# Kernel optimization log

Hardware: AMD Instinct MI355X
Metric: run time of the kernel (lower is better)

The kernel has to match this reference:

```python
import jax, jax.numpy as jnp
import numpy as np
from jax import lax

LEAK = 0.2   # LeakyReLU negative slope
EPS = 1e-5   # LayerNorm eps (torch default)
K = 16       # nsample

def _lrelu(x):
    return jnp.where(x > 0, x, LEAK * x)

def _ln(x, g, b):
    m = x.mean(-1, keepdims=True)
    v = x.var(-1, keepdims=True)
    return (x - m) / jnp.sqrt(v + EPS) * g + b

def _pointconv(xyz, new_xyz, feats, W, b):
    # xyz [B,N,3], new_xyz [B,M,3], feats [B,N,C] -> [B,M,O]
    d2 = (jnp.sum(new_xyz**2, -1)[:, :, None]
          + jnp.sum(xyz**2, -1)[:, None, :]
          - 2.0 * jnp.einsum('bmd,bnd->bmn', new_xyz, xyz))   # [B,M,N]
    _, idx = lax.top_k(-d2, K)                                # kNN indices [B,M,K]
    bidx = jnp.arange(xyz.shape[0])[:, None, None]
    g_xyz = xyz[bidx, idx] - new_xyz[:, :, None, :]           # relative coords [B,M,K,3]
    g_f = feats[bidx, idx]                                    # neighbor feats  [B,M,K,C]
    g = jnp.concatenate([g_xyz, g_f], -1)                     # [B,M,K,C+3]
    h = _lrelu(jnp.einsum('bmkc,co->bmko', g, W) + b)         # local MLP
    return h.max(2)                                           # max-pool over neighbors

def setup_inputs():
    key = jax.random.key(0)
    ks = jax.random.split(key, 8)
    B, N, base, C1 = 256, 1024, 16, 32
    def w(k, shape, fan):
        return jax.random.normal(k, shape, jnp.float32) * (1.0 / np.sqrt(fan))
    return dict(
        point_cloud=jax.random.normal(ks[0], (B, 3, N), jnp.float32),
        pw_W0=w(ks[1], (3, base), 3), pw_b0=jnp.zeros(base), pw_g0=jnp.ones(base), pw_beta0=jnp.zeros(base),
        pw_W1=w(ks[2], (base, base), base), pw_b1=jnp.zeros(base), pw_g1=jnp.ones(base), pw_beta1=jnp.zeros(base),
        pc0_W=w(ks[3], (base + 3, C1), base + 3), pc0_b=jnp.zeros(C1),
        bn_Ws=w(ks[4], (C1, C1 // 4), C1), bn_bs=jnp.zeros(C1 // 4),
        bn_Wc=w(ks[5], (C1 // 4 + 3, 128), C1 // 4 + 3), bn_bc=jnp.zeros(128),
        bn_We=w(ks[6], (128, 256), 128), bn_be=jnp.zeros(256),
    )

def reference(point_cloud, pw_W0, pw_b0, pw_g0, pw_beta0, pw_W1, pw_b1, pw_g1, pw_beta1,
              pc0_W, pc0_b, bn_Ws, bn_bs, bn_Wc, bn_bc, bn_We, bn_be):
    xyz0 = jnp.swapaxes(point_cloud, 1, 2)   # [B,1024,3]
    xyz1 = xyz0[:, ::2]                      # strided downsample -> [B,512,3]
    xyz2 = xyz1[:, ::4]                      # -> [B,128,3]
    # pointwise MLP (Linear-LN-LeakyReLU x2)
    f = _lrelu(_ln(xyz0 @ pw_W0 + pw_b0, pw_g0, pw_beta0))
    f = _lrelu(_ln(f @ pw_W1 + pw_b1, pw_g1, pw_beta1))       # [B,1024,16]
    # PointConv layer 0: 1024 -> 512 points, 16 -> 32 ch
    f = _pointconv(xyz0, xyz1, f, pc0_W, pc0_b)               # [B,512,32]
    # BottleneckStridedPointConv: squeeze (32->8), grouped conv (->128), expand (->256)
    fs = _lrelu(f @ bn_Ws + bn_bs)                            # [B,512,8]
    f = _pointconv(xyz1, xyz2, fs, bn_Wc, bn_bc)              # [B,128,128]
    f = f @ bn_We + bn_be                                     # [B,128,256]
    return f.mean(1)                                          # mean over points -> [B,256]
```

## Files before the change

### kernel.cpp

```cpp
#include <hip/hip_runtime.h>
#include <float.h>
#include <math.h>

#define LEAK 0.2f
#define EPS 1e-5f

__device__ __forceinline__ float lrelu(float v){ return v > 0.f ? v : LEAK*v; }

__device__ __forceinline__ void ln_lrelu16(float* h, const float* __restrict__ g, const float* __restrict__ be){
  float mu = 0.f;
#pragma unroll
  for (int o=0;o<16;o++) mu += h[o];
  mu *= 0.0625f;
  float var = 0.f;
#pragma unroll
  for (int o=0;o<16;o++){ float d = h[o]-mu; var += d*d; }
  var *= 0.0625f;
  float rs = 1.0f / sqrtf(var + EPS);
#pragma unroll
  for (int o=0;o<16;o++){ float v = (h[o]-mu)*rs*g[o] + be[o]; h[o] = lrelu(v); }
}

__global__ __launch_bounds__(256) void prep_kernel(const float* __restrict__ pc,
    const float* __restrict__ W0, const float* __restrict__ b0, const float* __restrict__ g0, const float* __restrict__ be0,
    const float* __restrict__ W1, const float* __restrict__ b1, const float* __restrict__ g1, const float* __restrict__ be1,
    float4* __restrict__ cand, float* __restrict__ feats)
{
  const int p = blockIdx.x*256 + threadIdx.x;
  const int b = p >> 10, n = p & 1023;
  const float* base = pc + b*3072;
  const float x = base[n], y = base[1024+n], z = base[2048+n];
  cand[p] = make_float4(x, y, z, x*x + y*y + z*z);
  float h[16];
#pragma unroll
  for (int o=0;o<16;o++) h[o] = b0[o] + x*W0[o] + y*W0[16+o] + z*W0[32+o];
  ln_lrelu16(h, g0, be0);
  float h2[16];
#pragma unroll
  for (int o=0;o<16;o++){
    float s = b1[o];
#pragma unroll
    for (int c=0;c<16;c++) s += h[c]*W1[c*16+o];
    h2[o] = s;
  }
  ln_lrelu16(h2, g1, be1);
  float4* fo = (float4*)(feats + p*16);
  fo[0] = make_float4(h2[0],h2[1],h2[2],h2[3]);
  fo[1] = make_float4(h2[4],h2[5],h2[6],h2[7]);
  fo[2] = make_float4(h2[8],h2[9],h2[10],h2[11]);
  fo[3] = make_float4(h2[12],h2[13],h2[14],h2[15]);
}

#define KNN_SENT 0xFF7FFC00u
__device__ __forceinline__ unsigned enc_key(float d, int n){
  unsigned u = __float_as_uint(d);
  u ^= (unsigned)(((int)u) >> 31) | 0x80000000u;
  return (u & ~1023u) | (unsigned)n;
}
__device__ __forceinline__ float dec_key(unsigned k){
  unsigned u = k ^ ((unsigned)(~(((int)k) >> 31)) | 0x80000000u);
  return __uint_as_float(u);
}

__device__ __forceinline__ unsigned med3u(unsigned a, unsigned b, unsigned c){
  unsigned d;
  asm("v_med3_u32 %0, %1, %2, %3" : "=v"(d) : "v"(a), "v"(b), "v"(c));
  return d;
}

__device__ __forceinline__ void ins_sorted(unsigned (&dk)[16], unsigned key){
#pragma unroll
  for (int j=15;j>0;--j) dk[j] = med3u(dk[j-1], dk[j], key);
  dk[0] = key < dk[0] ? key : dk[0];
}

template<int QS, int CS, int NQTOT, int NQ, int SPLIT, int NCAND>
__device__ __forceinline__ void knn_body(const float4* __restrict__ cand, int* __restrict__ idx_out)
{
  constexpr int NC = NCAND / SPLIT;
  constexpr int QG = NQTOT / NQ;
  constexpr int W  = SPLIT*NQ;
  __shared__ unsigned md[16*W];
  const int b = blockIdx.x / QG, qg = blockIdx.x % QG;
  const int tid = threadIdx.x;
  const int m = tid & (NQ-1), s = tid / NQ;
  const int mg = qg*NQ + m;
  const float4* __restrict__ cb = cand + b*1024;
  const float4 qv = cb[mg*QS];
  const float qx2=-2.f*qv.x, qy2=-2.f*qv.y, qz2=-2.f*qv.z;
  const int n0u = __builtin_amdgcn_readfirstlane(s*NC);

  unsigned dk[16];
#pragma unroll
  for (int j=0;j<16;j++) dk[j] = KNN_SENT;

#pragma unroll
  for (int t=0;t<16;t++){
    float4 c = cb[(n0u+t)*CS];
    float d = fmaf(c.x,qx2, fmaf(c.y,qy2, fmaf(c.z,qz2, c.w)));
    ins_sorted(dk, enc_key(d, n0u+t));
  }
  float Tf = dec_key(dk[15]);

  for (int ch=0; ch<NC/64; ch++){
    const int cb0u = n0u + ch*64;
    unsigned long long msk = 0ull;
    if (ch == 0){
#pragma unroll
      for (int t=16;t<64;t++){
        float4 c = cb[(cb0u+t)*CS];
        float d = fmaf(c.x,qx2, fmaf(c.y,qy2, fmaf(c.z,qz2, c.w)));
        if (d < Tf) msk |= (1ull<<t);
      }
    } else {
#pragma unroll 16
      for (int t=0;t<64;t++){
        float4 c = cb[(cb0u+t)*CS];
        float d = fmaf(c.x,qx2, fmaf(c.y,qy2, fmaf(c.z,qz2, c.w)));
        if (d < Tf) msk |= (1ull<<t);
      }
    }
    while (msk){
      const int t = __builtin_ctzll(msk);
      msk &= msk-1ull;
      float4 c = cb[(cb0u+t)*CS];
      float d = fmaf(c.x,qx2, fmaf(c.y,qy2, fmaf(c.z,qz2, c.w)));
      ins_sorted(dk, enc_key(d, cb0u+t));
    }
    Tf = dec_key(dk[15]);
  }

  if (s > 0){
    const int col = s*NQ + m;
#pragma unroll
    for (int j=0;j<16;j++) md[j*W + col] = dk[j];
  }
#pragma unroll
  for (int step = SPLIT/2; step > 1; step >>= 1){
    __syncthreads();
    if (s < step){
      const int col2 = (s+step)*NQ + m;
#pragma unroll
      for (int j=0;j<16;j++) ins_sorted(dk, md[j*W + col2]);
      if (s > 0){
        const int col = s*NQ + m;
#pragma unroll
        for (int j=0;j<16;j++) md[j*W + col] = dk[j];
      }
    }
  }
  __syncthreads();
  if (s == 0){
    const int col2 = NQ + m;
#pragma unroll
    for (int j=0;j<16;j++){
      unsigned o = md[(15-j)*W + col2];
      dk[j] = o < dk[j] ? o : dk[j];
    }
    int ik[16];
#pragma unroll
    for (int j=0;j<16;j++) ik[j] = (int)(dk[j] & 1023u);
    int4* op = (int4*)(idx_out + (b*NQTOT + mg)*16);
    op[0] = make_int4(ik[0],ik[1],ik[2],ik[3]);
    op[1] = make_int4(ik[4],ik[5],ik[6],ik[7]);
    op[2] = make_int4(ik[8],ik[9],ik[10],ik[11]);
    op[3] = make_int4(ik[12],ik[13],ik[14],ik[15]);
  }
}

__global__ __attribute__((amdgpu_flat_work_group_size(1024,1024), amdgpu_waves_per_eu(4,4)))
void knn1_kernel(const float4* __restrict__ cand, int* __restrict__ idx_out){
  knn_body<2,1,512,512,2,1024>(cand, idx_out);
}
__global__ __attribute__((amdgpu_flat_work_group_size(1024,1024), amdgpu_waves_per_eu(4,4)))
void knn2_kernel(const float4* __restrict__ cand, int* __restrict__ idx_out){
  knn_body<8,2,128,128,8,512>(cand, idx_out);
}

__global__ __attribute__((amdgpu_flat_work_group_size(512,512), amdgpu_waves_per_eu(2,2)))
void feat1_kernel(const float4* __restrict__ cand,
    const float* __restrict__ feats, const int* __restrict__ idx1,
    const float* __restrict__ W, const float* __restrict__ Wb,
    const float* __restrict__ Ws, const float* __restrict__ bs,
    float* __restrict__ fs_out)
{
  __shared__ float sP[1024*32];
  __shared__ float sx[1024], sy[1024], sz[1024];
  const int b = blockIdx.x, tid = threadIdx.x;
  const float4* __restrict__ cb = cand + b*1024;
  { float4 c0 = cb[tid], c1 = cb[tid+512];
    sx[tid]=c0.x; sy[tid]=c0.y; sz[tid]=c0.z;
    sx[tid+512]=c1.x; sy[tid+512]=c1.y; sz[tid+512]=c1.z; }

  const float4* __restrict__ fb4 = (const float4*)(feats + b*16384);
#pragma unroll
  for (int i=0;i<2;i++){
    const int j = tid + i*512;
    float4 f0 = fb4[j*4+0], f1 = fb4[j*4+1], f2 = fb4[j*4+2], f3 = fb4[j*4+3];
    float f[16] = {f0.x,f0.y,f0.z,f0.w, f1.x,f1.y,f1.z,f1.w,
                   f2.x,f2.y,f2.z,f2.w, f3.x,f3.y,f3.z,f3.w};
    float* row = sP + j*32;
    const int sw = (j & 7);
#pragma unroll
    for (int o4=0;o4<8;o4++){
      float4 s = *(const float4*)(Wb + o4*4);
#pragma unroll
      for (int c=0;c<16;c++){
        float4 w = *(const float4*)(W + (3+c)*32 + o4*4);
        s.x = fmaf(f[c], w.x, s.x);
        s.y = fmaf(f[c], w.y, s.y);
        s.z = fmaf(f[c], w.z, s.z);
        s.w = fmaf(f[c], w.w, s.w);
      }
      *(float4*)(row + ((o4 ^ sw) << 2)) = s;
    }
  }
  __syncthreads();

  const int m = tid;
  const float qx = sx[2*m], qy = sy[2*m], qz = sz[2*m];
  int idxr[16];
  { const int4* ip = (const int4*)(idx1 + (b*512+m)*16);
    int4 a=ip[0], b2=ip[1], c2=ip[2], d2=ip[3];
    idxr[0]=a.x; idxr[1]=a.y; idxr[2]=a.z; idxr[3]=a.w;
    idxr[4]=b2.x; idxr[5]=b2.y; idxr[6]=b2.z; idxr[7]=b2.w;
    idxr[8]=c2.x; idxr[9]=c2.y; idxr[10]=c2.z; idxr[11]=c2.w;
    idxr[12]=d2.x; idxr[13]=d2.y; idxr[14]=d2.z; idxr[15]=d2.w; }

  float w0[32], w1[32], w2[32];
#pragma unroll
  for (int o4=0;o4<8;o4++){
    float4 a = *(const float4*)(W +       o4*4);
    float4 bb= *(const float4*)(W + 32  + o4*4);
    float4 cc= *(const float4*)(W + 64  + o4*4);
    w0[o4*4]=a.x; w0[o4*4+1]=a.y; w0[o4*4+2]=a.z; w0[o4*4+3]=a.w;
    w1[o4*4]=bb.x; w1[o4*4+1]=bb.y; w1[o4*4+2]=bb.z; w1[o4*4+3]=bb.w;
    w2[o4*4]=cc.x; w2[o4*4+1]=cc.y; w2[o4*4+2]=cc.z; w2[o4*4+3]=cc.w;
  }

  float acc[32];
#pragma unroll
  for (int o=0;o<32;o++) acc[o] = -FLT_MAX;

#pragma unroll 4
  for (int k=0;k<16;k++){
    const int j = idxr[k];
    const float gx = sx[j]-qx, gy = sy[j]-qy, gz = sz[j]-qz;
    const float* row = sP + j*32;
    const int sw = (j & 7);
#pragma unroll
    for (int o4=0;o4<8;o4++){
      float4 p = *(const float4*)(row + ((o4 ^ sw) << 2));
      const int o0 = o4*4;
      float h0 = fmaf(gz, w2[o0+0], fmaf(gy, w1[o0+0], fmaf(gx, w0[o0+0], p.x)));
      float h1 = fmaf(gz, w2[o0+1], fmaf(gy, w1[o0+1], fmaf(gx, w0[o0+1], p.y)));
      float h2 = fmaf(gz, w2[o0+2], fmaf(gy, w1[o0+2], fmaf(gx, w0[o0+2], p.z)));
      float h3 = fmaf(gz, w2[o0+3], fmaf(gy, w1[o0+3], fmaf(gx, w0[o0+3], p.w)));
      acc[o0+0] = fmaxf(acc[o0+0], fmaxf(h0, 0.2f*h0));
      acc[o0+1] = fmaxf(acc[o0+1], fmaxf(h1, 0.2f*h1));
      acc[o0+2] = fmaxf(acc[o0+2], fmaxf(h2, 0.2f*h2));
      acc[o0+3] = fmaxf(acc[o0+3], fmaxf(h3, 0.2f*h3));
    }
  }

  float fsacc[8] = {0.f,0.f,0.f,0.f,0.f,0.f,0.f,0.f};
#pragma unroll
  for (int o=0;o<32;o++){
    const float a = acc[o];
    float4 u = *(const float4*)(Ws + o*8);
    float4 v = *(const float4*)(Ws + o*8 + 4);
    fsacc[0] = fmaf(a, u.x, fsacc[0]);
    fsacc[1] = fmaf(a, u.y, fsacc[1]);
    fsacc[2] = fmaf(a, u.z, fsacc[2]);
    fsacc[3] = fmaf(a, u.w, fsacc[3]);
    fsacc[4] = fmaf(a, v.x, fsacc[4]);
    fsacc[5] = fmaf(a, v.y, fsacc[5]);
    fsacc[6] = fmaf(a, v.z, fsacc[6]);
    fsacc[7] = fmaf(a, v.w, fsacc[7]);
  }
  float r[8];
#pragma unroll
  for (int p=0;p<8;p++) r[p] = lrelu(fsacc[p] + bs[p]);
  float4* op = (float4*)(fs_out + (b*512+m)*8);
  op[0] = make_float4(r[0],r[1],r[2],r[3]);
  op[1] = make_float4(r[4],r[5],r[6],r[7]);
}

__global__ __attribute__((amdgpu_flat_work_group_size(512,512), amdgpu_waves_per_eu(4,4)))
void feat2_kernel(const float4* __restrict__ cand,
    const float* __restrict__ fs, const int* __restrict__ idx2,
    const float* __restrict__ Wc, const float* __restrict__ bc,
    float* __restrict__ p2red)
{
  __shared__ float sP2[512*32];
  __shared__ float sx[512], sy[512], sz[512];
  __shared__ float sred[32];
  const int bx = blockIdx.x;
  const int b = bx >> 2, ob = bx & 3;
  const int o_base = ob*32;
  const int tid = threadIdx.x;

  const float4* __restrict__ cb = cand + b*1024;
  { float4 c0 = cb[2*tid];
    sx[tid]=c0.x; sy[tid]=c0.y; sz[tid]=c0.z; }
  if (tid < 32) sred[tid] = 0.f;

  { const float4* __restrict__ fj4 = (const float4*)(fs + b*4096 + tid*8);
    float4 fa = fj4[0], fb = fj4[1];
    float f[8] = {fa.x,fa.y,fa.z,fa.w, fb.x,fb.y,fb.z,fb.w};
    float* row = sP2 + tid*32;
    const int sw = (tid & 7);
#pragma unroll
    for (int o4=0;o4<8;o4++){
      float4 s = *(const float4*)(bc + o_base + o4*4);
#pragma unroll
      for (int c=0;c<8;c++){
        float4 w = *(const float4*)(Wc + (3+c)*128 + o_base + o4*4);
        s.x = fmaf(f[c], w.x, s.x);
        s.y = fmaf(f[c], w.y, s.y);
        s.z = fmaf(f[c], w.z, s.z);
        s.w = fmaf(f[c], w.w, s.w);
      }
      *(float4*)(row + ((o4 ^ sw) << 2)) = s;
    }
  }
  __syncthreads();

  const int m = tid >> 2, oq = tid & 3;
  const float qx = sx[4*m], qy = sy[4*m], qz = sz[4*m];
  int idxr[16];
  { const int4* ip = (const int4*)(idx2 + (b*128+m)*16);
    int4 a=ip[0], b2=ip[1], c2=ip[2], d2=ip[3];
    idxr[0]=a.x; idxr[1]=a.y; idxr[2]=a.z; idxr[3]=a.w;
    idxr[4]=b2.x; idxr[5]=b2.y; idxr[6]=b2.z; idxr[7]=b2.w;
    idxr[8]=c2.x; idxr[9]=c2.y; idxr[10]=c2.z; idxr[11]=c2.w;
    idxr[12]=d2.x; idxr[13]=d2.y; idxr[14]=d2.z; idxr[15]=d2.w; }

  float w0[8], w1[8], w2[8];
  { const int og = o_base + oq*8;
#pragma unroll
    for (int i=0;i<2;i++){
      float4 a = *(const float4*)(Wc +        og + i*4);
      float4 bb= *(const float4*)(Wc + 128  + og + i*4);
      float4 cc= *(const float4*)(Wc + 256  + og + i*4);
      w0[i*4]=a.x; w0[i*4+1]=a.y; w0[i*4+2]=a.z; w0[i*4+3]=a.w;
      w1[i*4]=bb.x; w1[i*4+1]=bb.y; w1[i*4+2]=bb.z; w1[i*4+3]=bb.w;
      w2[i*4]=cc.x; w2[i*4+1]=cc.y; w2[i*4+2]=cc.z; w2[i*4+3]=cc.w;
    } }

  float acc[8];
#pragma unroll
  for (int o=0;o<8;o++) acc[o] = -FLT_MAX;

#pragma unroll 4
  for (int k=0;k<16;k++){
    const int j = idxr[k];
    const float gx = sx[j]-qx, gy = sy[j]-qy, gz = sz[j]-qz;
    const float* row = sP2 + j*32;
    const int sw = (j & 7);
    float4 p0 = *(const float4*)(row + (((2*oq  ) ^ sw) << 2));
    float4 p1 = *(const float4*)(row + (((2*oq+1) ^ sw) << 2));
    float h0 = fmaf(gz, w2[0], fmaf(gy, w1[0], fmaf(gx, w0[0], p0.x)));
    float h1 = fmaf(gz, w2[1], fmaf(gy, w1[1], fmaf(gx, w0[1], p0.y)));
    float h2 = fmaf(gz, w2[2], fmaf(gy, w1[2], fmaf(gx, w0[2], p0.z)));
    float h3 = fmaf(gz, w2[3], fmaf(gy, w1[3], fmaf(gx, w0[3], p0.w)));
    float h4 = fmaf(gz, w2[4], fmaf(gy, w1[4], fmaf(gx, w0[4], p1.x)));
    float h5 = fmaf(gz, w2[5], fmaf(gy, w1[5], fmaf(gx, w0[5], p1.y)));
    float h6 = fmaf(gz, w2[6], fmaf(gy, w1[6], fmaf(gx, w0[6], p1.z)));
    float h7 = fmaf(gz, w2[7], fmaf(gy, w1[7], fmaf(gx, w0[7], p1.w)));
    acc[0] = fmaxf(acc[0], fmaxf(h0, 0.2f*h0));
    acc[1] = fmaxf(acc[1], fmaxf(h1, 0.2f*h1));
    acc[2] = fmaxf(acc[2], fmaxf(h2, 0.2f*h2));
    acc[3] = fmaxf(acc[3], fmaxf(h3, 0.2f*h3));
    acc[4] = fmaxf(acc[4], fmaxf(h4, 0.2f*h4));
    acc[5] = fmaxf(acc[5], fmaxf(h5, 0.2f*h5));
    acc[6] = fmaxf(acc[6], fmaxf(h6, 0.2f*h6));
    acc[7] = fmaxf(acc[7], fmaxf(h7, 0.2f*h7));
  }

#pragma unroll
  for (int o=0;o<8;o++){
    float v = acc[o];
    v += __shfl_xor(v, 4);
    v += __shfl_xor(v, 8);
    v += __shfl_xor(v, 16);
    v += __shfl_xor(v, 32);
    if ((threadIdx.x & 60) == 0)
      atomicAdd(&sred[oq*8+o], v);
  }
  __syncthreads();
  if (tid < 32) p2red[b*128 + o_base + tid] = sred[tid];
}

__global__ __launch_bounds__(256) void final_kernel(const float* __restrict__ p2red,
    const float* __restrict__ We, const float* __restrict__ beF, float* __restrict__ out)
{
  const int b = blockIdx.x, o = threadIdx.x;
  const float* __restrict__ r0 = p2red + b*128;
  float s = 0.f;
#pragma unroll 8
  for (int c=0;c<128;c++) s += r0[c]*We[c*256+o];
  out[b*256+o] = beF[o] + s*0.0078125f;
}

extern "C" void kernel_launch(void* const* d_in, const int* in_sizes, int n_in,
                              void* d_out, int out_size, void* d_ws, size_t ws_size,
                              hipStream_t stream) {
  (void)in_sizes; (void)n_in; (void)out_size; (void)ws_size;
  const float* pc   = (const float*)d_in[0];
  const float* W0   = (const float*)d_in[1];
  const float* b0   = (const float*)d_in[2];
  const float* g0   = (const float*)d_in[3];
  const float* be0  = (const float*)d_in[4];
  const float* W1   = (const float*)d_in[5];
  const float* b1   = (const float*)d_in[6];
  const float* g1   = (const float*)d_in[7];
  const float* be1  = (const float*)d_in[8];
  const float* pcW  = (const float*)d_in[9];
  const float* pcb  = (const float*)d_in[10];
  const float* Ws   = (const float*)d_in[11];
  const float* bs   = (const float*)d_in[12];
  const float* Wc   = (const float*)d_in[13];
  const float* bc   = (const float*)d_in[14];
  const float* We   = (const float*)d_in[15];
  const float* beF  = (const float*)d_in[16];

  char* ws = (char*)d_ws;
  float4* cand0 = (float4*)ws;
  float*  feats = (float*)(ws + (4u<<20));
  float*  p2red = (float*)(ws + (4u<<20));
  int*    idx1  = (int*)  (ws + (20u<<20));
  float*  fsb   = (float*)(ws + (28u<<20));
  int*    idx2  = (int*)  (ws + (32u<<20));
  float*  out   = (float*)d_out;

  prep_kernel<<<1024, 256, 0, stream>>>(pc, W0,b0,g0,be0, W1,b1,g1,be1, cand0, feats);
  knn1_kernel<<<256, 1024, 0, stream>>>(cand0, idx1);
  knn2_kernel<<<256, 1024, 0, stream>>>(cand0, idx2);
  feat1_kernel<<<256, 512, 0, stream>>>(cand0, feats, idx1, pcW, pcb, Ws, bs, fsb);
  feat2_kernel<<<1024, 512, 0, stream>>>(cand0, fsb, idx2, Wc, bc, p2red);
  final_kernel<<<256, 256, 0, stream>>>(p2red, We, beF, out);
}
```

Measured before the change: 252.7 us.

## Split feat1 output channels across two blocks and halve kNN chunk size

feat1 now splits its 32 output channels across two blocks per batch and stores the precomputed projections transposed in shared memory, which halves LDS use and allows higher occupancy. Each half writes a partial squeeze result, and feat2 sums the two partials and applies bias and LeakyReLU. kNN1 runs with 512-thread blocks covering half the queries each, and the kNN scan uses 32-candidate chunks with 32-bit masks so the threshold tightens more often. The cost is recomputed neighbor gathers, more global traffic for the partial sums, and possible LDS bank conflicts from scalar transposed reads.

```diff
diff --git a/kernel.cpp b/kernel.cpp
--- a/kernel.cpp
+++ b/kernel.cpp
@@ -102,27 +102,27 @@
   }
   float Tf = dec_key(dk[15]);
 
-  for (int ch=0; ch<NC/64; ch++){
-    const int cb0u = n0u + ch*64;
-    unsigned long long msk = 0ull;
+  for (int ch=0; ch<NC/32; ch++){
+    const int cb0u = n0u + ch*32;
+    unsigned msk = 0u;
     if (ch == 0){
 #pragma unroll
-      for (int t=16;t<64;t++){
+      for (int t=16;t<32;t++){
         float4 c = cb[(cb0u+t)*CS];
         float d = fmaf(c.x,qx2, fmaf(c.y,qy2, fmaf(c.z,qz2, c.w)));
-        if (d < Tf) msk |= (1ull<<t);
+        if (d < Tf) msk |= (1u<<t);
       }
     } else {
 #pragma unroll 16
-      for (int t=0;t<64;t++){
+      for (int t=0;t<32;t++){
         float4 c = cb[(cb0u+t)*CS];
         float d = fmaf(c.x,qx2, fmaf(c.y,qy2, fmaf(c.z,qz2, c.w)));
-        if (d < Tf) msk |= (1ull<<t);
+        if (d < Tf) msk |= (1u<<t);
       }
     }
     while (msk){
-      const int t = __builtin_ctzll(msk);
-      msk &= msk-1ull;
+      const int t = __builtin_ctz(msk);
+      msk &= msk-1u;
       float4 c = cb[(cb0u+t)*CS];
       float d = fmaf(c.x,qx2, fmaf(c.y,qy2, fmaf(c.z,qz2, c.w)));
       ins_sorted(dk, enc_key(d, cb0u+t));
@@ -168,25 +168,28 @@
   }
 }
 
-__global__ __attribute__((amdgpu_flat_work_group_size(1024,1024), amdgpu_waves_per_eu(4,4)))
+__global__ __attribute__((amdgpu_flat_work_group_size(512,512), amdgpu_waves_per_eu(4,4)))
 void knn1_kernel(const float4* __restrict__ cand, int* __restrict__ idx_out){
-  knn_body<2,1,512,512,2,1024>(cand, idx_out);
+  knn_body<2,1,512,256,2,1024>(cand, idx_out);
 }
 __global__ __attribute__((amdgpu_flat_work_group_size(1024,1024), amdgpu_waves_per_eu(4,4)))
 void knn2_kernel(const float4* __restrict__ cand, int* __restrict__ idx_out){
   knn_body<8,2,128,128,8,512>(cand, idx_out);
 }
 
-__global__ __attribute__((amdgpu_flat_work_group_size(512,512), amdgpu_waves_per_eu(2,2)))
+__global__ __attribute__((amdgpu_flat_work_group_size(512,512), amdgpu_waves_per_eu(4,4)))
 void feat1_kernel(const float4* __restrict__ cand,
     const float* __restrict__ feats, const int* __restrict__ idx1,
     const float* __restrict__ W, const float* __restrict__ Wb,
-    const float* __restrict__ Ws, const float* __restrict__ bs,
-    float* __restrict__ fs_out)
+    const float* __restrict__ Ws,
+    float* __restrict__ p1part)
 {
-  __shared__ float sP[1024*32];
+  __shared__ float sPT[16*1024];
   __shared__ float sx[1024], sy[1024], sz[1024];
-  const int b = blockIdx.x, tid = threadIdx.x;
+  const int bx = blockIdx.x;
+  const int b = bx >> 1, ob = bx & 1;
+  const int ob16 = ob*16;
+  const int tid = threadIdx.x;
   const float4* __restrict__ cb = cand + b*1024;
   { float4 c0 = cb[tid], c1 = cb[tid+512];
     sx[tid]=c0.x; sy[tid]=c0.y; sz[tid]=c0.z;
@@ -199,20 +202,21 @@
     float4 f0 = fb4[j*4+0], f1 = fb4[j*4+1], f2 = fb4[j*4+2], f3 = fb4[j*4+3];
     float f[16] = {f0.x,f0.y,f0.z,f0.w, f1.x,f1.y,f1.z,f1.w,
                    f2.x,f2.y,f2.z,f2.w, f3.x,f3.y,f3.z,f3.w};
-    float* row = sP + j*32;
-    const int sw = (j & 7);
-#pragma unroll
-    for (int o4=0;o4<8;o4++){
-      float4 s = *(const float4*)(Wb + o4*4);
+#pragma unroll
+    for (int o4=0;o4<4;o4++){
+      float4 s = *(const float4*)(Wb + ob16 + o4*4);
 #pragma unroll
       for (int c=0;c<16;c++){
-        float4 w = *(const float4*)(W + (3+c)*32 + o4*4);
+        float4 w = *(const float4*)(W + (3+c)*32 + ob16 + o4*4);
         s.x = fmaf(f[c], w.x, s.x);
         s.y = fmaf(f[c], w.y, s.y);
         s.z = fmaf(f[c], w.z, s.z);
         s.w = fmaf(f[c], w.w, s.w);
       }
-      *(float4*)(row + ((o4 ^ sw) << 2)) = s;
+      sPT[(o4*4+0)*1024 + j] = s.x;
+      sPT[(o4*4+1)*1024 + j] = s.y;
+      sPT[(o4*4+2)*1024 + j] = s.z;
+      sPT[(o4*4+3)*1024 + j] = s.w;
     }
   }
   __syncthreads();
@@ -227,48 +231,40 @@
     idxr[8]=c2.x; idxr[9]=c2.y; idxr[10]=c2.z; idxr[11]=c2.w;
     idxr[12]=d2.x; idxr[13]=d2.y; idxr[14]=d2.z; idxr[15]=d2.w; }
 
-  float w0[32], w1[32], w2[32];
-#pragma unroll
-  for (int o4=0;o4<8;o4++){
-    float4 a = *(const float4*)(W +       o4*4);
-    float4 bb= *(const float4*)(W + 32  + o4*4);
-    float4 cc= *(const float4*)(W + 64  + o4*4);
-    w0[o4*4]=a.x; w0[o4*4+1]=a.y; w0[o4*4+2]=a.z; w0[o4*4+3]=a.w;
-    w1[o4*4]=bb.x; w1[o4*4+1]=bb.y; w1[o4*4+2]=bb.z; w1[o4*4+3]=bb.w;
-    w2[o4*4]=cc.x; w2[o4*4+1]=cc.y; w2[o4*4+2]=cc.z; w2[o4*4+3]=cc.w;
-  }
-
-  float acc[32];
-#pragma unroll
-  for (int o=0;o<32;o++) acc[o] = -FLT_MAX;
+  float w0[16], w1[16], w2[16];
+#pragma unroll
+  for (int i=0;i<4;i++){
+    float4 a = *(const float4*)(W +       ob16 + i*4);
+    float4 bb= *(const float4*)(W + 32  + ob16 + i*4);
+    float4 cc= *(const float4*)(W + 64  + ob16 + i*4);
+    w0[i*4]=a.x; w0[i*4+1]=a.y; w0[i*4+2]=a.z; w0[i*4+3]=a.w;
+    w1[i*4]=bb.x; w1[i*4+1]=bb.y; w1[i*4+2]=bb.z; w1[i*4+3]=bb.w;
+    w2[i*4]=cc.x; w2[i*4+1]=cc.y; w2[i*4+2]=cc.z; w2[i*4+3]=cc.w;
+  }
+
+  float acc[16];
+#pragma unroll
+  for (int o=0;o<16;o++) acc[o] = -FLT_MAX;
 
 #pragma unroll 4
   for (int k=0;k<16;k++){
     const int j = idxr[k];
     const float gx = sx[j]-qx, gy = sy[j]-qy, gz = sz[j]-qz;
-    const float* row = sP + j*32;
-    const int sw = (j & 7);
-#pragma unroll
-    for (int o4=0;o4<8;o4++){
-      float4 p = *(const float4*)(row + ((o4 ^ sw) << 2));
-      const int o0 = o4*4;
-      float h0 = fmaf(gz, w2[o0+0], fmaf(gy, w1[o0+0], fmaf(gx, w0[o0+0], p.x)));
-      float h1 = fmaf(gz, w2[o0+1], fmaf(gy, w1[o0+1], fmaf(gx, w0[o0+1], p.y)));
-      float h2 = fmaf(gz, w2[o0+2], fmaf(gy, w1[o0+2], fmaf(gx, w0[o0+2], p.z)));
-      float h3 = fmaf(gz, w2[o0+3], fmaf(gy, w1[o0+3], fmaf(gx, w0[o0+3], p.w)));
-      acc[o0+0] = fmaxf(acc[o0+0], fmaxf(h0, 0.2f*h0));
-      acc[o0+1] = fmaxf(acc[o0+1], fmaxf(h1, 0.2f*h1));
-      acc[o0+2] = fmaxf(acc[o0+2], fmaxf(h2, 0.2f*h2));
-      acc[o0+3] = fmaxf(acc[o0+3], fmaxf(h3, 0.2f*h3));
+    const float* pj = sPT + j;
+#pragma unroll
+    for (int o=0;o<16;o++){
+      float p = pj[o*1024];
+      float h = fmaf(gz, w2[o], fmaf(gy, w1[o], fmaf(gx, w0[o], p)));
+      acc[o] = fmaxf(acc[o], fmaxf(h, 0.2f*h));
     }
   }
 
   float fsacc[8] = {0.f,0.f,0.f,0.f,0.f,0.f,0.f,0.f};
 #pragma unroll
-  for (int o=0;o<32;o++){
+  for (int o=0;o<16;o++){
     const float a = acc[o];
-    float4 u = *(const float4*)(Ws + o*8);
-    float4 v = *(const float4*)(Ws + o*8 + 4);
+    float4 u = *(const float4*)(Ws + (ob16+o)*8);
+    float4 v = *(const float4*)(Ws + (ob16+o)*8 + 4);
     fsacc[0] = fmaf(a, u.x, fsacc[0]);
     fsacc[1] = fmaf(a, u.y, fsacc[1]);
     fsacc[2] = fmaf(a, u.z, fsacc[2]);
@@ -278,18 +274,16 @@
     fsacc[6] = fmaf(a, v.z, fsacc[6]);
     fsacc[7] = fmaf(a, v.w, fsacc[7]);
   }
-  float r[8];
-#pragma unroll
-  for (int p=0;p<8;p++) r[p] = lrelu(fsacc[p] + bs[p]);
-  float4* op = (float4*)(fs_out + (b*512+m)*8);
-  op[0] = make_float4(r[0],r[1],r[2],r[3]);
-  op[1] = make_float4(r[4],r[5],r[6],r[7]);
+  float4* op = (float4*)(p1part + ((b*2+ob)*512 + m)*8);
+  op[0] = make_float4(fsacc[0],fsacc[1],fsacc[2],fsacc[3]);
+  op[1] = make_float4(fsacc[4],fsacc[5],fsacc[6],fsacc[7]);
 }
 
 __global__ __attribute__((amdgpu_flat_work_group_size(512,512), amdgpu_waves_per_eu(4,4)))
 void feat2_kernel(const float4* __restrict__ cand,
-    const float* __restrict__ fs, const int* __restrict__ idx2,
+    const float* __restrict__ p1part, const int* __restrict__ idx2,
     const float* __restrict__ Wc, const float* __restrict__ bc,
+    const float* __restrict__ bs,
     float* __restrict__ p2red)
 {
   __shared__ float sP2[512*32];
@@ -305,9 +299,15 @@
     sx[tid]=c0.x; sy[tid]=c0.y; sz[tid]=c0.z; }
   if (tid < 32) sred[tid] = 0.f;
 
-  { const float4* __restrict__ fj4 = (const float4*)(fs + b*4096 + tid*8);
-    float4 fa = fj4[0], fb = fj4[1];
-    float f[8] = {fa.x,fa.y,fa.z,fa.w, fb.x,fb.y,fb.z,fb.w};
+  { const float4* __restrict__ pa4 = (const float4*)(p1part + ((b*2+0)*512 + tid)*8);
+    const float4* __restrict__ pb4 = (const float4*)(p1part + ((b*2+1)*512 + tid)*8);
+    float4 a0 = pa4[0], a1 = pa4[1], c0 = pb4[0], c1 = pb4[1];
+    float4 s0 = *(const float4*)(bs), s1 = *(const float4*)(bs+4);
+    float f[8];
+    f[0]=lrelu(a0.x+c0.x+s0.x); f[1]=lrelu(a0.y+c0.y+s0.y);
+    f[2]=lrelu(a0.z+c0.z+s0.z); f[3]=lrelu(a0.w+c0.w+s0.w);
+    f[4]=lrelu(a1.x+c1.x+s1.x); f[5]=lrelu(a1.y+c1.y+s1.y);
+    f[6]=lrelu(a1.z+c1.z+s1.z); f[7]=lrelu(a1.w+c1.w+s1.w);
     float* row = sP2 + tid*32;
     const int sw = (tid & 7);
 #pragma unroll
@@ -430,14 +430,14 @@
   float*  feats = (float*)(ws + (4u<<20));
   float*  p2red = (float*)(ws + (4u<<20));
   int*    idx1  = (int*)  (ws + (20u<<20));
-  float*  fsb   = (float*)(ws + (28u<<20));
-  int*    idx2  = (int*)  (ws + (32u<<20));
+  int*    idx2  = (int*)  (ws + (28u<<20));
+  float*  p1part= (float*)(ws + (30u<<20));
   float*  out   = (float*)d_out;
 
   prep_kernel<<<1024, 256, 0, stream>>>(pc, W0,b0,g0,be0, W1,b1,g1,be1, cand0, feats);
-  knn1_kernel<<<256, 1024, 0, stream>>>(cand0, idx1);
+  knn1_kernel<<<512, 512, 0, stream>>>(cand0, idx1);
   knn2_kernel<<<256, 1024, 0, stream>>>(cand0, idx2);
-  feat1_kernel<<<256, 512, 0, stream>>>(cand0, feats, idx1, pcW, pcb, Ws, bs, fsb);
-  feat2_kernel<<<1024, 512, 0, stream>>>(cand0, fsb, idx2, Wc, bc, p2red);
+  feat1_kernel<<<512, 512, 0, stream>>>(cand0, feats, idx1, pcW, pcb, Ws, p1part);
+  feat2_kernel<<<1024, 512, 0, stream>>>(cand0, p1part, idx2, Wc, bc, bs, p2red);
   final_kernel<<<256, 256, 0, stream>>>(p2red, We, beF, out);
 }
```

Result: slower. 258.6 us (+2.3%).
